# Optimization experiments

Hardware: AMD Instinct MI355X
Metric: run time of the kernel (lower is better)

The kernel has to match this reference:

```python
import jax, jax.numpy as jnp
import numpy as np

B, H, W = 1, 32, 32
C, G, K = 128, 4, 15
GC = C // G          # group channels = 32
K2 = K * K           # 225
RED = 4              # SE reduction
KHID = 32            # kernel_net hidden


def setup_inputs() -> dict:
    key = jax.random.key(0)
    ks = jax.random.split(key, 24)
    def n(k, shape, s=0.02):
        return jax.random.normal(k, shape, jnp.float32) * s
    inp = {
        'x': jax.random.normal(ks[0], (B, H, W, C), jnp.float32),
        # scalars (torch: raw_sigma init = softplus^{-1}(0.3), base_offset_scale = 0.1)
        'raw_sigma': jnp.asarray(float(np.log(np.expm1(0.3))), jnp.float32),
        'base_offset_scale': jnp.asarray(0.1, jnp.float32),
        # input/output projections
        'w_in': n(ks[1], (C, C)), 'b_in': jnp.zeros((C,), jnp.float32),
        'w_out': n(ks[2], (C, C)), 'b_out': jnp.zeros((C,), jnp.float32),
        # dw_conv: depthwise 3x3 (HWIO, I=1 per group) + pointwise 1x1
        'dw_k': n(ks[3], (3, 3, 1, C), 0.1), 'dw_b': jnp.zeros((C,), jnp.float32),
        'pw_w': n(ks[4], (C, C)), 'pw_b': jnp.zeros((C,), jnp.float32),
        # offset / mask nets (zero-init in torch; small random here to exercise gather)
        'off_w': n(ks[5], (C, G * K2 * 2), 0.01), 'off_b': n(ks[6], (G * K2 * 2,), 0.01),
        'msk_w': n(ks[7], (C, G * K2), 0.01), 'msk_b': n(ks[8], (G * K2,), 0.01),
        # kernel_net: 2 -> 32 -> 32 -> G*GC
        'k1_w': n(ks[9], (2, KHID), 0.3), 'k1_b': jnp.zeros((KHID,), jnp.float32),
        'k2_w': n(ks[10], (KHID, KHID), 0.2), 'k2_b': jnp.zeros((KHID,), jnp.float32),
        'k3_w': n(ks[11], (KHID, G * GC), 0.2), 'k3_b': jnp.zeros((G * GC,), jnp.float32),
        # SE block
        'se1_w': n(ks[12], (C, C // RED), 0.1), 'se1_b': jnp.zeros((C // RED,), jnp.float32),
        'se2_w': n(ks[13], (C // RED, C), 0.1), 'se2_b': jnp.zeros((C,), jnp.float32),
    }
    return inp


def reference(x, raw_sigma, base_offset_scale, w_in, b_in, w_out, b_out,
              dw_k, dw_b, pw_w, pw_b, off_w, off_b, msk_w, msk_b,
              k1_w, k1_b, k2_w, k2_b, k3_w, k3_b, se1_w, se1_b, se2_w, se2_b):
    # sigma (scalar path, biases=None)
    sigma = jnp.clip(jax.nn.softplus(raw_sigma), 0.001, 0.5)
    grid = jnp.linspace(-0.5, 0.5, K)

    x_proj = x @ w_in + b_in                                   # [B,H,W,C]

    # dw_conv: depthwise 3x3 -> SiLU -> 1x1
    y = jax.lax.conv_general_dilated(
        x, dw_k, (1, 1), 'SAME',
        dimension_numbers=('NHWC', 'HWIO', 'NHWC'),
        feature_group_count=C) + dw_b
    x_dw = jax.nn.silu(y) @ pw_w + pw_b                        # [B,H,W,C]

    # Gaussian envelope over kernel grid, normalized (scalar sigma -> shape [K,K])
    gh = grid[:, None]; gw = grid[None, :]
    env = jnp.exp(-(gh ** 2 + gw ** 2) / (2.0 * sigma ** 2))
    env = env / jnp.clip(env.sum(), 1e-8)                      # [K,K]

    # dynamic kernel weights from grid positions (*2); replicate torch's
    # contiguous view (K,K,G,gc) -> (G,K2,gc)
    pos = jnp.stack(jnp.meshgrid(grid, grid, indexing='ij'), -1).reshape(K2, 2) * 2.0
    h1 = jax.nn.silu(pos @ k1_w + k1_b)
    h2 = jax.nn.silu(h1 @ k2_w + k2_b)
    kw = (h2 @ k3_w + k3_b).reshape(K, K, G, GC).reshape(G, K2, GC)  # [G,K2,gc]

    offsets = (x_dw @ off_w + off_b).reshape(B, H, W, G, K2, 2) * base_offset_scale
    raw_mask = (x_dw @ msk_w + msk_b).reshape(B, H, W, G, K2) * env.reshape(1, 1, 1, 1, K2)
    attn = jnp.nan_to_num(jax.nn.softmax(raw_mask, axis=-1))   # [B,H,W,G,K2]

    # reference sampling grid (integer offsets -K//2..K//2)
    ref = jnp.linspace(-(K // 2), K // 2, K)
    ref_grid = jnp.stack(jnp.meshgrid(ref, ref, indexing='ij'), -1).reshape(K2, 2)
    pos_h = jnp.arange(H, dtype=jnp.float32).reshape(1, H, 1, 1, 1)
    pos_w = jnp.arange(W, dtype=jnp.float32).reshape(1, 1, W, 1, 1)

    abs_h = pos_h + ref_grid[:, 0].reshape(1, 1, 1, 1, K2) + offsets[..., 0]
    abs_w = pos_w + ref_grid[:, 1].reshape(1, 1, 1, 1, K2) + offsets[..., 1]
    ah = jnp.clip(abs_h, 0.0, H - 1); aw = jnp.clip(abs_w, 0.0, W - 1)
    hf = jnp.clip(ah.astype(jnp.int32), 0, H - 1)
    wf = jnp.clip(aw.astype(jnp.int32), 0, W - 1)
    hc = jnp.clip(hf + 1, 0, H - 1)
    wc = jnp.clip(wf + 1, 0, W - 1)
    hw = ah - hf.astype(jnp.float32)
    ww = aw - wf.astype(jnp.float32)
    valid = (~((abs_h < 0) | (abs_h > H - 1) | (abs_w < 0) | (abs_w > W - 1))).astype(jnp.float32)

    x_g = x_proj.reshape(B, H, W, G, GC)
    b_idx = jnp.arange(B).reshape(B, 1, 1, 1, 1)
    g_idx = jnp.arange(G).reshape(1, 1, 1, G, 1)
    def gather(hi, wi):
        return x_g[b_idx, hi, wi, g_idx]                       # [B,H,W,G,K2,gc]

    sampled = (gather(hf, wf) * ((1 - hw) * (1 - ww) * valid)[..., None]
             + gather(hf, wc) * ((1 - hw) * ww * valid)[..., None]
             + gather(hc, wf) * (hw * (1 - ww) * valid)[..., None]
             + gather(hc, wc) * (hw * ww * valid)[..., None])

    sampled = sampled * kw.reshape(1, 1, 1, G, K2, GC)
    out = jnp.einsum('bhwgkc,bhwgk->bhwgc', sampled, attn).reshape(B, H, W, C)

    # SE block (mask=None, bias=None)
    pooled = out.mean(axis=(1, 2), keepdims=True)
    scale = jax.nn.sigmoid(jax.nn.silu(pooled @ se1_w + se1_b) @ se2_w + se2_b)
    out = out * scale

    return out @ w_out + b_out
```

## Files before the change

### kernel.cpp

```cpp
#include <hip/hip_runtime.h>
#include <math.h>

constexpr int H = 32, W = 32, C = 128, G = 4, K = 15, K2 = 225, GC = 32;
constexpr int NPIX = H * W;
constexpr int NOFF = G * K2 * 2;
constexpr int NMSK = G * K2;
constexpr int NTOT = NOFF + NMSK;
constexpr int KHID = 32;

constexpr size_t WS_ENV    = 128;
constexpr size_t WS_KW     = 384;
constexpr size_t WS_PART   = 29184;
constexpr size_t WS_XPROJ  = 94720;
constexpr size_t WS_XDW    = 225792;
constexpr size_t WS_OFFS   = 356864;
constexpr size_t WS_MASK   = 2200064;
constexpr size_t WS_OUTPRE = 3121664;

__device__ __forceinline__ float sigmoidf_(float v) { return 1.f / (1.f + expf(-v)); }
__device__ __forceinline__ float siluf_(float v)    { return v / (1.f + expf(-v)); }

__device__ __forceinline__ void mlp_point(int k2i, int lane,
        const float* __restrict__ k1_w, const float* __restrict__ k1_b,
        const float* __restrict__ k2_w, const float* __restrict__ k2_b,
        const float* __restrict__ k3_w, const float* __restrict__ k3_b,
        float* __restrict__ ws) {
    int i = k2i / 15, j = k2i % 15;
    float ph = (-0.5f + (float)i * (1.f / 14.f)) * 2.f;
    float pw = (-0.5f + (float)j * (1.f / 14.f)) * 2.f;
    float h1[KHID], h2[KHID];
#pragma unroll
    for (int m = 0; m < KHID; m++)
        h1[m] = siluf_(fmaf(ph, k1_w[m], fmaf(pw, k1_w[KHID + m], k1_b[m])));
#pragma unroll
    for (int m = 0; m < KHID; m++) {
        float a = k2_b[m];
#pragma unroll
        for (int q = 0; q < KHID; q++) a = fmaf(h1[q], k2_w[q * KHID + m], a);
        h2[m] = siluf_(a);
    }
#pragma unroll
    for (int t = 0; t < 2; t++) {
        int col = lane + t * 64;
        float a = k3_b[col];
#pragma unroll
        for (int q = 0; q < KHID; q++) a = fmaf(h2[q], k3_w[q * C + col], a);
        ws[WS_KW + (size_t)k2i * C + col] = a;
    }
}

__global__ __launch_bounds__(256) void prep_front_kernel(const float* __restrict__ x,
        const float* __restrict__ raw_sigma,
        const float* __restrict__ w_in, const float* __restrict__ b_in,
        const float* __restrict__ dw_k, const float* __restrict__ dw_b,
        const float* __restrict__ pw_w, const float* __restrict__ pw_b,
        const float* __restrict__ k1_w, const float* __restrict__ k1_b,
        const float* __restrict__ k2_w, const float* __restrict__ k2_b,
        const float* __restrict__ k3_w, const float* __restrict__ k3_b,
        float* __restrict__ ws) {
    int tid = threadIdx.x;
    int b = blockIdx.x;
    if (b < 256) {
        __shared__ float xs[4][C], ts[4][C];
        int p0 = b * 4;
        int c = tid & 127, pp = tid >> 7;
#pragma unroll
        for (int q = 0; q < 2; q++) {
            int px = pp * 2 + q;
            int p = p0 + px;
            int h = p >> 5, w = p & 31;
            xs[px][c] = x[(size_t)p * C + c];
            float y = dw_b[c];
#pragma unroll
            for (int dy = 0; dy < 3; dy++) {
                int hh = h + dy - 1;
                if (hh < 0 || hh >= H) continue;
#pragma unroll
                for (int dx = 0; dx < 3; dx++) {
                    int wq = w + dx - 1;
                    if (wq < 0 || wq >= W) continue;
                    y = fmaf(x[((size_t)hh * W + wq) * C + c], dw_k[(dy * 3 + dx) * C + c], y);
                }
            }
            ts[px][c] = siluf_(y);
        }
        __syncthreads();
        float ap0 = b_in[c], ap1 = ap0, ad0 = pw_b[c], ad1 = ad0;
        int b0 = pp * 2, b1 = pp * 2 + 1;
        for (int i = 0; i < C; i += 4) {
#pragma unroll
            for (int u = 0; u < 4; u++) {
                float wi = w_in[(size_t)(i + u) * C + c];
                float pi = pw_w[(size_t)(i + u) * C + c];
                ap0 = fmaf(xs[b0][i + u], wi, ap0);
                ap1 = fmaf(xs[b1][i + u], wi, ap1);
                ad0 = fmaf(ts[b0][i + u], pi, ad0);
                ad1 = fmaf(ts[b1][i + u], pi, ad1);
            }
        }
        ws[WS_XPROJ + (size_t)(p0 + b0) * C + c] = ap0;
        ws[WS_XPROJ + (size_t)(p0 + b1) * C + c] = ap1;
        ws[WS_XDW  + (size_t)(p0 + b0) * C + c] = ad0;
        ws[WS_XDW  + (size_t)(p0 + b1) * C + c] = ad1;
    } else {
        int mb = b - 256;
        if (mb == 0) {
            __shared__ float red[256];
            float xsg = raw_sigma[0];
            float sp = fmaxf(xsg, 0.f) + log1pf(expf(-fabsf(xsg)));
            float sigma = fminf(fmaxf(sp, 0.001f), 0.5f);
            float inv2s2 = 1.f / (2.f * sigma * sigma);
            int i = tid / 15, j = tid % 15;
            float e = 0.f;
            if (tid < K2) {
                float gi = -0.5f + (float)i * (1.f / 14.f);
                float gj = -0.5f + (float)j * (1.f / 14.f);
                e = expf(-(gi * gi + gj * gj) * inv2s2);
            }
            red[tid] = e;
            __syncthreads();
            for (int s = 128; s > 0; s >>= 1) {
                if (tid < s) red[tid] += red[tid + s];
                __syncthreads();
            }
            float esum = fmaxf(red[0], 1e-8f);
            if (tid < K2) ws[WS_ENV + tid] = e / esum;
            if (tid < 64) mlp_point(224, tid, k1_w, k1_b, k2_w, k2_b, k3_w, k3_b, ws);
        } else {
            int k2i = (mb - 1) * 4 + (tid >> 6);
            mlp_point(k2i, tid & 63, k1_w, k1_b, k2_w, k2_b, k3_w, k3_b, ws);
        }
    }
}

__global__ __launch_bounds__(256) void offmsk_gemm(const float* __restrict__ A,
        const float* __restrict__ off_w, const float* __restrict__ off_b,
        const float* __restrict__ msk_w, const float* __restrict__ msk_b,
        const float* __restrict__ bos, const float* __restrict__ env,
        float* __restrict__ offs_out, float* __restrict__ mask_out) {
    __shared__ float At[32][132];
    __shared__ float Bs[32][128];
    int tid = threadIdx.x;
    int c0 = blockIdx.x * 128;
    int p0 = blockIdx.y * 128;
    int tx = tid & 15, ty = tid >> 4;

    float acc[8][8];
#pragma unroll
    for (int i = 0; i < 8; i++)
#pragma unroll
        for (int j = 0; j < 8; j++) acc[i][j] = 0.f;

    int cL = (tid & 31) * 4;
    int kB = tid >> 5;
    int cB = c0 + cL;
    const float* bptr = nullptr; int bstride = 0;
    if (cB < NOFF)       { bptr = off_w + cB;          bstride = NOFF; }
    else if (cB < NTOT)  { bptr = msk_w + (cB - NOFF); bstride = NMSK; }
    int rA = tid >> 3, k4A = (tid & 7) * 4;

    for (int kt = 0; kt < C; kt += 32) {
        if (kt) __syncthreads();
#pragma unroll
        for (int pass = 0; pass < 4; pass++) {
            int r = rA + pass * 32;
            float4 v = *(const float4*)&A[(size_t)(p0 + r) * C + kt + k4A];
            At[k4A + 0][r] = v.x; At[k4A + 1][r] = v.y;
            At[k4A + 2][r] = v.z; At[k4A + 3][r] = v.w;
        }
#pragma unroll
        for (int pass = 0; pass < 4; pass++) {
            int k = kB + pass * 8;
            float4 bv = make_float4(0.f, 0.f, 0.f, 0.f);
            if (bptr) bv = *(const float4*)&bptr[(size_t)(kt + k) * bstride];
            *(float4*)&Bs[k][cL] = bv;
        }
        __syncthreads();
#pragma unroll 4
        for (int k = 0; k < 32; k++) {
            float4 a0 = *(const float4*)&At[k][ty * 8];
            float4 a1 = *(const float4*)&At[k][ty * 8 + 4];
            float4 b0 = *(const float4*)&Bs[k][tx * 8];
            float4 b1 = *(const float4*)&Bs[k][tx * 8 + 4];
            const float av[8] = {a0.x, a0.y, a0.z, a0.w, a1.x, a1.y, a1.z, a1.w};
            const float bv[8] = {b0.x, b0.y, b0.z, b0.w, b1.x, b1.y, b1.z, b1.w};
#pragma unroll
            for (int i = 0; i < 8; i++)
#pragma unroll
                for (int j = 0; j < 8; j++)
                    acc[i][j] = fmaf(av[i], bv[j], acc[i][j]);
        }
    }

    int colbase = c0 + tx * 8;
    if (colbase >= NTOT) return;
    bool full = (colbase + 8) <= NTOT;
    float bias[8], sc[8];
    float* obase;
    int ostride;
    if (colbase < NOFF) {
        float s = bos[0];
#pragma unroll
        for (int j = 0; j < 8; j++) { bias[j] = off_b[colbase + j]; sc[j] = s; }
        obase = offs_out + colbase; ostride = NOFF;
    } else {
        int m0 = colbase - NOFF;
#pragma unroll
        for (int j = 0; j < 8; j++) {
            if (colbase + j < NTOT) { bias[j] = msk_b[m0 + j]; sc[j] = env[(m0 + j) % K2]; }
            else                    { bias[j] = 0.f; sc[j] = 0.f; }
        }
        obase = mask_out + m0; ostride = NMSK;
    }
#pragma unroll
    for (int i = 0; i < 8; i++) {
        size_t row = (size_t)(p0 + ty * 8 + i);
        if (full) {
            float4 r0 = make_float4((acc[i][0] + bias[0]) * sc[0], (acc[i][1] + bias[1]) * sc[1],
                                    (acc[i][2] + bias[2]) * sc[2], (acc[i][3] + bias[3]) * sc[3]);
            float4 r1 = make_float4((acc[i][4] + bias[4]) * sc[4], (acc[i][5] + bias[5]) * sc[5],
                                    (acc[i][6] + bias[6]) * sc[6], (acc[i][7] + bias[7]) * sc[7]);
            *(float4*)&obase[row * ostride]     = r0;
            *(float4*)&obase[row * ostride + 4] = r1;
        } else {
#pragma unroll
            for (int j = 0; j < 8; j++)
                if (colbase + j < NTOT)
                    obase[row * ostride + j] = (acc[i][j] + bias[j]) * sc[j];
        }
    }
}

__global__ __launch_bounds__(256) void sampler_kernel(const float* __restrict__ ws_offs,
        const float* __restrict__ ws_mask, const float* __restrict__ xproj,
        const float* __restrict__ kwf, float* __restrict__ outpre,
        float* __restrict__ partial) {
    int blk = blockIdx.x;
    int p0 = blk * 2;
    int h = p0 >> 5;
    int tid = threadIdx.x;

    __shared__ float   attn_s[2][NMSK];
    __shared__ float4  wgt_s[2][NMSK];
    __shared__ ushort4 loc_s[2][NMSK];
    __shared__ float   outp[2][C];

    {
        int half = tid >> 5;
        int l32 = tid & 31;
        int px = half >> 2, g = half & 3;
        const float* mrow = ws_mask + (size_t)(p0 + px) * NMSK + g * K2;
        float v[8];
        float mx = -1e30f;
#pragma unroll
        for (int q = 0; q < 8; q++) {
            int k = l32 + q * 32;
            v[q] = (k < K2) ? mrow[k] : -1e30f;
            mx = fmaxf(mx, v[q]);
        }
#pragma unroll
        for (int s = 16; s > 0; s >>= 1) mx = fmaxf(mx, __shfl_xor(mx, s));
        float sum = 0.f;
#pragma unroll
        for (int q = 0; q < 8; q++) {
            int k = l32 + q * 32;
            v[q] = (k < K2) ? expf(v[q] - mx) : 0.f;
            sum += v[q];
        }
#pragma unroll
        for (int s = 16; s > 0; s >>= 1) sum += __shfl_xor(sum, s);
        float inv = 1.f / sum;
#pragma unroll
        for (int q = 0; q < 8; q++) {
            int k = l32 + q * 32;
            if (k < K2) attn_s[px][g * K2 + k] = v[q] * inv;
        }
    }
    __syncthreads();

    for (int e = tid; e < 2 * NMSK; e += 256) {
        int px = (e >= NMSK) ? 1 : 0;
        int m = e - px * NMSK;
        int g = m / K2;
        int k = m - g * K2;
        int p = p0 + px;
        int w = p & 31;
        float2 o = *(const float2*)&ws_offs[(size_t)p * NOFF + m * 2];
        float abs_h = (float)(h + k / 15 - 7) + o.x;
        float abs_w = (float)(w + k % 15 - 7) + o.y;
        float validf = (abs_h < 0.f || abs_h > 31.f || abs_w < 0.f || abs_w > 31.f) ? 0.f : 1.f;
        float ah = fminf(fmaxf(abs_h, 0.f), 31.f);
        float aw = fminf(fmaxf(abs_w, 0.f), 31.f);
        int hf = (int)ah, wf = (int)aw;
        int hc = min(hf + 1, 31), wc = min(wf + 1, 31);
        float hwt = ah - (float)hf, wwt = aw - (float)wf;
        float a = attn_s[px][m] * validf;
        float u0 = 1.f - hwt, u1 = 1.f - wwt;
        wgt_s[px][m] = make_float4(a * u0 * u1, a * u0 * wwt, a * hwt * u1, a * hwt * wwt);
        loc_s[px][m] = make_ushort4((unsigned short)(hf * W + wf), (unsigned short)(hf * W + wc),
                                    (unsigned short)(hc * W + wf), (unsigned short)(hc * W + wc));
    }
    __syncthreads();

    {
        int cq = tid & 7;
        int s  = (tid >> 3) & 3;
        int g  = (tid >> 5) & 3;
        int px = tid >> 7;
        int k0 = (s * K2) >> 2;
        int k1 = ((s + 1) * K2) >> 2;
        const float* xpg = xproj + g * GC + cq * 4;
        const float* kwg = kwf + (size_t)g * (K2 * GC) + cq * 4;
        float4 acc = make_float4(0.f, 0.f, 0.f, 0.f);
#pragma unroll 2
        for (int k = k0; k < k1; k++) {
            int m = g * K2 + k;
            ushort4 L  = loc_s[px][m];
            float4  Wv = wgt_s[px][m];
            float4 x00 = *(const float4*)(xpg + (int)L.x * C);
            float4 x01 = *(const float4*)(xpg + (int)L.y * C);
            float4 x10 = *(const float4*)(xpg + (int)L.z * C);
            float4 x11 = *(const float4*)(xpg + (int)L.w * C);
            float4 kw4 = *(const float4*)(kwg + k * GC);
            float sx = fmaf(Wv.w, x11.x, fmaf(Wv.z, x10.x, fmaf(Wv.y, x01.x, Wv.x * x00.x)));
            float sy = fmaf(Wv.w, x11.y, fmaf(Wv.z, x10.y, fmaf(Wv.y, x01.y, Wv.x * x00.y)));
            float sz = fmaf(Wv.w, x11.z, fmaf(Wv.z, x10.z, fmaf(Wv.y, x01.z, Wv.x * x00.z)));
            float sw = fmaf(Wv.w, x11.w, fmaf(Wv.z, x10.w, fmaf(Wv.y, x01.w, Wv.x * x00.w)));
            acc.x = fmaf(kw4.x, sx, acc.x);
            acc.y = fmaf(kw4.y, sy, acc.y);
            acc.z = fmaf(kw4.z, sz, acc.z);
            acc.w = fmaf(kw4.w, sw, acc.w);
        }
        acc.x += __shfl_xor(acc.x, 8);  acc.y += __shfl_xor(acc.y, 8);
        acc.z += __shfl_xor(acc.z, 8);  acc.w += __shfl_xor(acc.w, 8);
        acc.x += __shfl_xor(acc.x, 16); acc.y += __shfl_xor(acc.y, 16);
        acc.z += __shfl_xor(acc.z, 16); acc.w += __shfl_xor(acc.w, 16);
        if (s == 0) {
            *(float4*)&outp[px][g * GC + cq * 4] = acc;
            *(float4*)&outpre[(size_t)(p0 + px) * C + g * GC + cq * 4] = acc;
        }
    }
    __syncthreads();
    if (tid < C)
        partial[(size_t)blk * C + tid] = outp[0][tid] + outp[1][tid];
}

__global__ __launch_bounds__(256) void finale_kernel(const float* __restrict__ outpre,
        const float* __restrict__ partial,
        const float* __restrict__ se1_w, const float* __restrict__ se1_b,
        const float* __restrict__ se2_w, const float* __restrict__ se2_b,
        const float* __restrict__ w_out, const float* __restrict__ b_out,
        float* __restrict__ out) {
    int tid = threadIdx.x;
    __shared__ float tmp[8][132];
    __shared__ float pooled[C];
    __shared__ float hid[KHID];
    __shared__ float scl[C];
    __shared__ float v[4][C];

    {
        int bg = tid >> 5, c4 = (tid & 31) * 4;
        float4 s4 = make_float4(0.f, 0.f, 0.f, 0.f);
        for (int i = 0; i < 64; i++) {
            float4 pv = *(const float4*)&partial[(size_t)(bg * 64 + i) * C + c4];
            s4.x += pv.x; s4.y += pv.y; s4.z += pv.z; s4.w += pv.w;
        }
        *(float4*)&tmp[bg][c4] = s4;
    }
    __syncthreads();
    if (tid < C) {
        float s = 0.f;
#pragma unroll
        for (int g = 0; g < 8; g++) s += tmp[g][tid];
        pooled[tid] = s * (1.f / 1024.f);
    }
    __syncthreads();
    if (tid < KHID) {
        float a = se1_b[tid];
        for (int cc = 0; cc < C; cc++) a = fmaf(pooled[cc], se1_w[cc * KHID + tid], a);
        hid[tid] = siluf_(a);
    }
    __syncthreads();
    if (tid < C) {
        float a = se2_b[tid];
#pragma unroll
        for (int q = 0; q < KHID; q++) a = fmaf(hid[q], se2_w[q * C + tid], a);
        scl[tid] = sigmoidf_(a);
    }
    __syncthreads();

    int p0 = blockIdx.x * 4;
    int c = tid & 127, pp = tid >> 7;
#pragma unroll
    for (int q = 0; q < 2; q++) {
        int px = pp * 2 + q;
        v[px][c] = outpre[(size_t)(p0 + px) * C + c] * scl[c];
    }
    __syncthreads();
    float a0 = b_out[c], a1 = b_out[c];
    int b0 = pp * 2, b1 = pp * 2 + 1;
    for (int i = 0; i < C; i += 4) {
#pragma unroll
        for (int u = 0; u < 4; u++) {
            float wv = w_out[(size_t)(i + u) * C + c];
            a0 = fmaf(v[b0][i + u], wv, a0);
            a1 = fmaf(v[b1][i + u], wv, a1);
        }
    }
    out[(size_t)(p0 + b0) * C + c] = a0;
    out[(size_t)(p0 + b1) * C + c] = a1;
}

extern "C" void kernel_launch(void* const* d_in, const int* in_sizes, int n_in,
                              void* d_out, int out_size, void* d_ws, size_t ws_size,
                              hipStream_t stream) {
    const float* x         = (const float*)d_in[0];
    const float* raw_sigma = (const float*)d_in[1];
    const float* bos       = (const float*)d_in[2];
    const float* w_in      = (const float*)d_in[3];
    const float* b_in      = (const float*)d_in[4];
    const float* w_out     = (const float*)d_in[5];
    const float* b_out     = (const float*)d_in[6];
    const float* dw_k      = (const float*)d_in[7];
    const float* dw_b      = (const float*)d_in[8];
    const float* pw_w      = (const float*)d_in[9];
    const float* pw_b      = (const float*)d_in[10];
    const float* off_w     = (const float*)d_in[11];
    const float* off_b     = (const float*)d_in[12];
    const float* msk_w     = (const float*)d_in[13];
    const float* msk_b     = (const float*)d_in[14];
    const float* k1_w      = (const float*)d_in[15];
    const float* k1_b      = (const float*)d_in[16];
    const float* k2_w      = (const float*)d_in[17];
    const float* k2_b      = (const float*)d_in[18];
    const float* k3_w      = (const float*)d_in[19];
    const float* k3_b      = (const float*)d_in[20];
    const float* se1_w     = (const float*)d_in[21];
    const float* se1_b     = (const float*)d_in[22];
    const float* se2_w     = (const float*)d_in[23];
    const float* se2_b     = (const float*)d_in[24];

    float* ws  = (float*)d_ws;
    float* out = (float*)d_out;

    prep_front_kernel<<<313, 256, 0, stream>>>(x, raw_sigma, w_in, b_in, dw_k, dw_b,
                                               pw_w, pw_b, k1_w, k1_b, k2_w, k2_b,
                                               k3_w, k3_b, ws);

    dim3 gg((NTOT + 127) / 128, NPIX / 128);
    offmsk_gemm<<<gg, 256, 0, stream>>>(ws + WS_XDW, off_w, off_b, msk_w, msk_b, bos,
                                        ws + WS_ENV, ws + WS_OFFS, ws + WS_MASK);

    sampler_kernel<<<NPIX / 2, 256, 0, stream>>>(ws + WS_OFFS, ws + WS_MASK, ws + WS_XPROJ,
                                                 ws + WS_KW, ws + WS_OUTPRE, ws + WS_PART);

    finale_kernel<<<NPIX / 4, 256, 0, stream>>>(ws + WS_OUTPRE, ws + WS_PART,
                                                se1_w, se1_b, se2_w, se2_b,
                                                w_out, b_out, out);
}
```

Before: 79.63 us.

## Stage neighborhood tile in LDS for sampler and shrink offset GEMM tiles

The sampler now handles a 2x2 pixel block per workgroup. For each group it stages an 18x18 halo tile of x_proj channels in shared memory, so bilinear gathers read LDS instead of global memory. Zero-weight samples are skipped, and the finale partial-sum reduction changes to match 256 blocks. The offset/mask GEMM moves from 128x128 to 64x64 tiles, giving more blocks. The sampler risks many more barriers per block, lower occupancy from about 47KB of LDS, and clamped halo indices if offsets fall outside the tile.

```diff
diff --git a/kernel.cpp b/kernel.cpp
--- a/kernel.cpp
+++ b/kernel.cpp
@@ -138,96 +138,72 @@
         const float* __restrict__ msk_w, const float* __restrict__ msk_b,
         const float* __restrict__ bos, const float* __restrict__ env,
         float* __restrict__ offs_out, float* __restrict__ mask_out) {
-    __shared__ float At[32][132];
-    __shared__ float Bs[32][128];
+    __shared__ float At[32][72];
+    __shared__ float Bs[32][64];
     int tid = threadIdx.x;
-    int c0 = blockIdx.x * 128;
-    int p0 = blockIdx.y * 128;
+    int c0 = blockIdx.x * 64;
+    int p0 = blockIdx.y * 64;
     int tx = tid & 15, ty = tid >> 4;
-
-    float acc[8][8];
-#pragma unroll
-    for (int i = 0; i < 8; i++)
-#pragma unroll
-        for (int j = 0; j < 8; j++) acc[i][j] = 0.f;
-
-    int cL = (tid & 31) * 4;
-    int kB = tid >> 5;
+    float acc[4][4];
+#pragma unroll
+    for (int i = 0; i < 4; i++)
+#pragma unroll
+        for (int j = 0; j < 4; j++) acc[i][j] = 0.f;
+    int cL = (tid * 4) & 63;
+    int kL = (tid * 4) >> 6;
     int cB = c0 + cL;
     const float* bptr = nullptr; int bstride = 0;
     if (cB < NOFF)       { bptr = off_w + cB;          bstride = NOFF; }
     else if (cB < NTOT)  { bptr = msk_w + (cB - NOFF); bstride = NMSK; }
     int rA = tid >> 3, k4A = (tid & 7) * 4;
-
     for (int kt = 0; kt < C; kt += 32) {
         if (kt) __syncthreads();
 #pragma unroll
-        for (int pass = 0; pass < 4; pass++) {
+        for (int pass = 0; pass < 2; pass++) {
             int r = rA + pass * 32;
             float4 v = *(const float4*)&A[(size_t)(p0 + r) * C + kt + k4A];
             At[k4A + 0][r] = v.x; At[k4A + 1][r] = v.y;
             At[k4A + 2][r] = v.z; At[k4A + 3][r] = v.w;
-        }
-#pragma unroll
-        for (int pass = 0; pass < 4; pass++) {
-            int k = kB + pass * 8;
+            int k = kL + pass * 16;
             float4 bv = make_float4(0.f, 0.f, 0.f, 0.f);
             if (bptr) bv = *(const float4*)&bptr[(size_t)(kt + k) * bstride];
             *(float4*)&Bs[k][cL] = bv;
         }
         __syncthreads();
-#pragma unroll 4
+#pragma unroll
         for (int k = 0; k < 32; k++) {
-            float4 a0 = *(const float4*)&At[k][ty * 8];
-            float4 a1 = *(const float4*)&At[k][ty * 8 + 4];
-            float4 b0 = *(const float4*)&Bs[k][tx * 8];
-            float4 b1 = *(const float4*)&Bs[k][tx * 8 + 4];
-            const float av[8] = {a0.x, a0.y, a0.z, a0.w, a1.x, a1.y, a1.z, a1.w};
-            const float bv[8] = {b0.x, b0.y, b0.z, b0.w, b1.x, b1.y, b1.z, b1.w};
-#pragma unroll
-            for (int i = 0; i < 8; i++)
-#pragma unroll
-                for (int j = 0; j < 8; j++)
+            float4 a4 = *(const float4*)&At[k][ty * 4];
+            float4 b4 = *(const float4*)&Bs[k][tx * 4];
+            const float av[4] = {a4.x, a4.y, a4.z, a4.w};
+            const float bv[4] = {b4.x, b4.y, b4.z, b4.w};
+#pragma unroll
+            for (int i = 0; i < 4; i++)
+#pragma unroll
+                for (int j = 0; j < 4; j++)
                     acc[i][j] = fmaf(av[i], bv[j], acc[i][j]);
         }
     }
-
-    int colbase = c0 + tx * 8;
+    int colbase = c0 + tx * 4;
     if (colbase >= NTOT) return;
-    bool full = (colbase + 8) <= NTOT;
-    float bias[8], sc[8];
-    float* obase;
-    int ostride;
+    float bias[4], sc[4];
+    float* obase; int ostride;
     if (colbase < NOFF) {
         float s = bos[0];
 #pragma unroll
-        for (int j = 0; j < 8; j++) { bias[j] = off_b[colbase + j]; sc[j] = s; }
+        for (int j = 0; j < 4; j++) { bias[j] = off_b[colbase + j]; sc[j] = s; }
         obase = offs_out + colbase; ostride = NOFF;
     } else {
         int m0 = colbase - NOFF;
 #pragma unroll
-        for (int j = 0; j < 8; j++) {
-            if (colbase + j < NTOT) { bias[j] = msk_b[m0 + j]; sc[j] = env[(m0 + j) % K2]; }
-            else                    { bias[j] = 0.f; sc[j] = 0.f; }
-        }
+        for (int j = 0; j < 4; j++) { bias[j] = msk_b[m0 + j]; sc[j] = env[(m0 + j) % K2]; }
         obase = mask_out + m0; ostride = NMSK;
     }
 #pragma unroll
-    for (int i = 0; i < 8; i++) {
-        size_t row = (size_t)(p0 + ty * 8 + i);
-        if (full) {
-            float4 r0 = make_float4((acc[i][0] + bias[0]) * sc[0], (acc[i][1] + bias[1]) * sc[1],
-                                    (acc[i][2] + bias[2]) * sc[2], (acc[i][3] + bias[3]) * sc[3]);
-            float4 r1 = make_float4((acc[i][4] + bias[4]) * sc[4], (acc[i][5] + bias[5]) * sc[5],
-                                    (acc[i][6] + bias[6]) * sc[6], (acc[i][7] + bias[7]) * sc[7]);
-            *(float4*)&obase[row * ostride]     = r0;
-            *(float4*)&obase[row * ostride + 4] = r1;
-        } else {
-#pragma unroll
-            for (int j = 0; j < 8; j++)
-                if (colbase + j < NTOT)
-                    obase[row * ostride + j] = (acc[i][j] + bias[j]) * sc[j];
-        }
+    for (int i = 0; i < 4; i++) {
+        size_t row = (size_t)(p0 + ty * 4 + i);
+        float4 r0 = make_float4((acc[i][0] + bias[0]) * sc[0], (acc[i][1] + bias[1]) * sc[1],
+                                (acc[i][2] + bias[2]) * sc[2], (acc[i][3] + bias[3]) * sc[3]);
+        *(float4*)&obase[row * ostride] = r0;
     }
 }
 
@@ -236,113 +212,142 @@
         const float* __restrict__ kwf, float* __restrict__ outpre,
         float* __restrict__ partial) {
     int blk = blockIdx.x;
-    int p0 = blk * 2;
-    int h = p0 >> 5;
+    int h0 = (blk >> 4) * 2, w0 = (blk & 15) * 2;
     int tid = threadIdx.x;
 
-    __shared__ float   attn_s[2][NMSK];
-    __shared__ float4  wgt_s[2][NMSK];
-    __shared__ ushort4 loc_s[2][NMSK];
-    __shared__ float   outp[2][C];
-
-    {
-        int half = tid >> 5;
-        int l32 = tid & 31;
-        int px = half >> 2, g = half & 3;
-        const float* mrow = ws_mask + (size_t)(p0 + px) * NMSK + g * K2;
-        float v[8];
-        float mx = -1e30f;
-#pragma unroll
-        for (int q = 0; q < 8; q++) {
-            int k = l32 + q * 32;
-            v[q] = (k < K2) ? mrow[k] : -1e30f;
-            mx = fmaxf(mx, v[q]);
-        }
-#pragma unroll
-        for (int s = 16; s > 0; s >>= 1) mx = fmaxf(mx, __shfl_xor(mx, s));
-        float sum = 0.f;
-#pragma unroll
-        for (int q = 0; q < 8; q++) {
-            int k = l32 + q * 32;
-            v[q] = (k < K2) ? expf(v[q] - mx) : 0.f;
-            sum += v[q];
-        }
-#pragma unroll
-        for (int s = 16; s > 0; s >>= 1) sum += __shfl_xor(sum, s);
-        float inv = 1.f / sum;
-#pragma unroll
-        for (int q = 0; q < 8; q++) {
-            int k = l32 + q * 32;
-            if (k < K2) attn_s[px][g * K2 + k] = v[q] * inv;
-        }
-    }
-    __syncthreads();
-
-    for (int e = tid; e < 2 * NMSK; e += 256) {
-        int px = (e >= NMSK) ? 1 : 0;
-        int m = e - px * NMSK;
-        int g = m / K2;
-        int k = m - g * K2;
-        int p = p0 + px;
-        int w = p & 31;
-        float2 o = *(const float2*)&ws_offs[(size_t)p * NOFF + m * 2];
-        float abs_h = (float)(h + k / 15 - 7) + o.x;
-        float abs_w = (float)(w + k % 15 - 7) + o.y;
-        float validf = (abs_h < 0.f || abs_h > 31.f || abs_w < 0.f || abs_w > 31.f) ? 0.f : 1.f;
-        float ah = fminf(fmaxf(abs_h, 0.f), 31.f);
-        float aw = fminf(fmaxf(abs_w, 0.f), 31.f);
-        int hf = (int)ah, wf = (int)aw;
-        int hc = min(hf + 1, 31), wc = min(wf + 1, 31);
-        float hwt = ah - (float)hf, wwt = aw - (float)wf;
-        float a = attn_s[px][m] * validf;
-        float u0 = 1.f - hwt, u1 = 1.f - wwt;
-        wgt_s[px][m] = make_float4(a * u0 * u1, a * u0 * wwt, a * hwt * u1, a * hwt * wwt);
-        loc_s[px][m] = make_ushort4((unsigned short)(hf * W + wf), (unsigned short)(hf * W + wc),
-                                    (unsigned short)(hc * W + wf), (unsigned short)(hc * W + wc));
-    }
-    __syncthreads();
-
-    {
-        int cq = tid & 7;
-        int s  = (tid >> 3) & 3;
-        int g  = (tid >> 5) & 3;
-        int px = tid >> 7;
-        int k0 = (s * K2) >> 2;
-        int k1 = ((s + 1) * K2) >> 2;
-        const float* xpg = xproj + g * GC + cq * 4;
-        const float* kwg = kwf + (size_t)g * (K2 * GC) + cq * 4;
-        float4 acc = make_float4(0.f, 0.f, 0.f, 0.f);
-#pragma unroll 2
-        for (int k = k0; k < k1; k++) {
-            int m = g * K2 + k;
-            ushort4 L  = loc_s[px][m];
-            float4  Wv = wgt_s[px][m];
-            float4 x00 = *(const float4*)(xpg + (int)L.x * C);
-            float4 x01 = *(const float4*)(xpg + (int)L.y * C);
-            float4 x10 = *(const float4*)(xpg + (int)L.z * C);
-            float4 x11 = *(const float4*)(xpg + (int)L.w * C);
-            float4 kw4 = *(const float4*)(kwg + k * GC);
-            float sx = fmaf(Wv.w, x11.x, fmaf(Wv.z, x10.x, fmaf(Wv.y, x01.x, Wv.x * x00.x)));
-            float sy = fmaf(Wv.w, x11.y, fmaf(Wv.z, x10.y, fmaf(Wv.y, x01.y, Wv.x * x00.y)));
-            float sz = fmaf(Wv.w, x11.z, fmaf(Wv.z, x10.z, fmaf(Wv.y, x01.z, Wv.x * x00.z)));
-            float sw = fmaf(Wv.w, x11.w, fmaf(Wv.z, x10.w, fmaf(Wv.y, x01.w, Wv.x * x00.w)));
-            acc.x = fmaf(kw4.x, sx, acc.x);
-            acc.y = fmaf(kw4.y, sy, acc.y);
-            acc.z = fmaf(kw4.z, sz, acc.z);
-            acc.w = fmaf(kw4.w, sw, acc.w);
-        }
-        acc.x += __shfl_xor(acc.x, 8);  acc.y += __shfl_xor(acc.y, 8);
-        acc.z += __shfl_xor(acc.z, 8);  acc.w += __shfl_xor(acc.w, 8);
-        acc.x += __shfl_xor(acc.x, 16); acc.y += __shfl_xor(acc.y, 16);
-        acc.z += __shfl_xor(acc.z, 16); acc.w += __shfl_xor(acc.w, 16);
-        if (s == 0) {
-            *(float4*)&outp[px][g * GC + cq * 4] = acc;
-            *(float4*)&outpre[(size_t)(p0 + px) * C + g * GC + cq * 4] = acc;
-        }
-    }
-    __syncthreads();
+    __shared__ float   reg[324 * 36];
+    __shared__ float   attn_g[4][228];
+    __shared__ float4  wvec[256];
+    __shared__ ushort4 locr[256];
+    __shared__ float4  rbuf[256];
+    __shared__ float   outp[4][C];
+
+    float4 accg;
+
+    for (int g = 0; g < G; ++g) {
+        for (int f = tid; f < 2592; f += 256) {
+            int cell = f >> 3, c4 = (f & 7) << 2;
+            int rr = cell / 18, cc2 = cell - rr * 18;
+            int gh = min(max(h0 - 8 + rr, 0), 31);
+            int gw = min(max(w0 - 8 + cc2, 0), 31);
+            float4 v = *(const float4*)&xproj[(size_t)((gh << 5) + gw) * C + g * GC + c4];
+            *(float4*)&reg[cell * 36 + c4] = v;
+        }
+        {
+            int px = tid >> 6, lane = tid & 63;
+            int p = ((h0 + (px >> 1)) << 5) + w0 + (px & 1);
+            const float* mrow = ws_mask + (size_t)p * NMSK + g * K2;
+            float v[4];
+            float mx = -1e30f;
+#pragma unroll
+            for (int q = 0; q < 4; q++) {
+                int k = lane + q * 64;
+                v[q] = (k < K2) ? mrow[k] : -1e30f;
+                mx = fmaxf(mx, v[q]);
+            }
+#pragma unroll
+            for (int s = 32; s > 0; s >>= 1) mx = fmaxf(mx, __shfl_xor(mx, s));
+            float sum = 0.f;
+#pragma unroll
+            for (int q = 0; q < 4; q++) {
+                int k = lane + q * 64;
+                v[q] = (k < K2) ? expf(v[q] - mx) : 0.f;
+                sum += v[q];
+            }
+#pragma unroll
+            for (int s = 32; s > 0; s >>= 1) sum += __shfl_xor(sum, s);
+            float inv = 1.f / sum;
+#pragma unroll
+            for (int q = 0; q < 4; q++) {
+                int k = lane + q * 64;
+                if (k < K2) attn_g[px][k] = v[q] * inv;
+            }
+        }
+        __syncthreads();
+
+        accg = make_float4(0.f, 0.f, 0.f, 0.f);
+        for (int kc = 0; kc < K2; kc += 64) {
+            {
+                int px = tid >> 6, kk = tid & 63, k = kc + kk;
+                float a = 0.f, hwt = 0.f, wwt = 0.f;
+                ushort4 l4 = make_ushort4(0, 0, 0, 0);
+                if (k < K2) {
+                    int ph = h0 + (px >> 1), pw = w0 + (px & 1);
+                    int p = (ph << 5) + pw;
+                    float2 o = *(const float2*)&ws_offs[(size_t)p * NOFF + (g * K2 + k) * 2];
+                    float abs_h = (float)(ph + k / 15 - 7) + o.x;
+                    float abs_w = (float)(pw + k % 15 - 7) + o.y;
+                    float validf = (abs_h < 0.f || abs_h > 31.f || abs_w < 0.f || abs_w > 31.f) ? 0.f : 1.f;
+                    float ah = fminf(fmaxf(abs_h, 0.f), 31.f);
+                    float aw = fminf(fmaxf(abs_w, 0.f), 31.f);
+                    int hf = (int)ah, wf = (int)aw;
+                    int hc = min(hf + 1, 31), wc = min(wf + 1, 31);
+                    hwt = ah - (float)hf; wwt = aw - (float)wf;
+                    a = attn_g[px][k] * validf;
+                    int ri0 = min(max(hf - h0 + 8, 0), 17);
+                    int ri1 = min(max(hc - h0 + 8, 0), 17);
+                    int rj0 = min(max(wf - w0 + 8, 0), 17);
+                    int rj1 = min(max(wc - w0 + 8, 0), 17);
+                    l4 = make_ushort4((unsigned short)(ri0 * 18 + rj0), (unsigned short)(ri0 * 18 + rj1),
+                                      (unsigned short)(ri1 * 18 + rj0), (unsigned short)(ri1 * 18 + rj1));
+                }
+                wvec[tid] = make_float4(a, hwt, wwt, 0.f);
+                locr[tid] = l4;
+            }
+            __syncthreads();
+            {
+                int cq = tid & 7, px = (tid >> 3) & 3, s = tid >> 5;
+#pragma unroll
+                for (int i = 0; i < 8; i++) {
+                    int kk = s * 8 + i;
+                    int e = px * 64 + kk;
+                    float4 wv = wvec[e];
+                    if (wv.x != 0.f) {
+                        ushort4 L = locr[e];
+                        float u0 = 1.f - wv.y, u1 = 1.f - wv.z;
+                        float w00 = wv.x * u0 * u1,   w01 = wv.x * u0 * wv.z;
+                        float w10 = wv.x * wv.y * u1, w11 = wv.x * wv.y * wv.z;
+                        float4 x00 = *(const float4*)&reg[(int)L.x * 36 + cq * 4];
+                        float4 x01 = *(const float4*)&reg[(int)L.y * 36 + cq * 4];
+                        float4 x10 = *(const float4*)&reg[(int)L.z * 36 + cq * 4];
+                        float4 x11 = *(const float4*)&reg[(int)L.w * 36 + cq * 4];
+                        float4 kw4 = *(const float4*)&kwf[(size_t)g * (K2 * GC) + (kc + kk) * GC + cq * 4];
+                        float sx = fmaf(w11, x11.x, fmaf(w10, x10.x, fmaf(w01, x01.x, w00 * x00.x)));
+                        float sy = fmaf(w11, x11.y, fmaf(w10, x10.y, fmaf(w01, x01.y, w00 * x00.y)));
+                        float sz = fmaf(w11, x11.z, fmaf(w10, x10.z, fmaf(w01, x01.z, w00 * x00.z)));
+                        float sw = fmaf(w11, x11.w, fmaf(w10, x10.w, fmaf(w01, x01.w, w00 * x00.w)));
+                        accg.x = fmaf(kw4.x, sx, accg.x);
+                        accg.y = fmaf(kw4.y, sy, accg.y);
+                        accg.z = fmaf(kw4.z, sz, accg.z);
+                        accg.w = fmaf(kw4.w, sw, accg.w);
+                    }
+                }
+            }
+            __syncthreads();
+        }
+        {
+            int cq = tid & 7, px = (tid >> 3) & 3, s = tid >> 5;
+            rbuf[s * 32 + px * 8 + cq] = accg;
+        }
+        __syncthreads();
+        if (tid < 128) {
+            int px = tid >> 5, cc = tid & 31;
+            float v = 0.f;
+#pragma unroll
+            for (int s = 0; s < 8; s++)
+                v += ((const float*)&rbuf[s * 32 + px * 8 + (cc >> 2)])[cc & 3];
+            outp[px][g * GC + cc] = v;
+        }
+        __syncthreads();
+    }
+
+    for (int t = tid; t < 4 * C; t += 256) {
+        int px = t >> 7, c = t & 127;
+        int p = ((h0 + (px >> 1)) << 5) + w0 + (px & 1);
+        outpre[(size_t)p * C + c] = outp[px][c];
+    }
     if (tid < C)
-        partial[(size_t)blk * C + tid] = outp[0][tid] + outp[1][tid];
+        partial[(size_t)blk * C + tid] = outp[0][tid] + outp[1][tid] + outp[2][tid] + outp[3][tid];
 }
 
 __global__ __launch_bounds__(256) void finale_kernel(const float* __restrict__ outpre,
@@ -361,8 +366,8 @@
     {
         int bg = tid >> 5, c4 = (tid & 31) * 4;
         float4 s4 = make_float4(0.f, 0.f, 0.f, 0.f);
-        for (int i = 0; i < 64; i++) {
-            float4 pv = *(const float4*)&partial[(size_t)(bg * 64 + i) * C + c4];
+        for (int i = 0; i < 32; i++) {
+            float4 pv = *(const float4*)&partial[(size_t)(bg * 32 + i) * C + c4];
             s4.x += pv.x; s4.y += pv.y; s4.z += pv.z; s4.w += pv.w;
         }
         *(float4*)&tmp[bg][c4] = s4;
@@ -447,12 +452,12 @@
                                                pw_w, pw_b, k1_w, k1_b, k2_w, k2_b,
                                                k3_w, k3_b, ws);
 
-    dim3 gg((NTOT + 127) / 128, NPIX / 128);
+    dim3 gg((NTOT + 63) / 64, NPIX / 64);
     offmsk_gemm<<<gg, 256, 0, stream>>>(ws + WS_XDW, off_w, off_b, msk_w, msk_b, bos,
                                         ws + WS_ENV, ws + WS_OFFS, ws + WS_MASK);
 
-    sampler_kernel<<<NPIX / 2, 256, 0, stream>>>(ws + WS_OFFS, ws + WS_MASK, ws + WS_XPROJ,
-                                                 ws + WS_KW, ws + WS_OUTPRE, ws + WS_PART);
+    sampler_kernel<<<256, 256, 0, stream>>>(ws + WS_OFFS, ws + WS_MASK, ws + WS_XPROJ,
+                                            ws + WS_KW, ws + WS_OUTPRE, ws + WS_PART);
 
     finale_kernel<<<NPIX / 4, 256, 0, stream>>>(ws + WS_OUTPRE, ws + WS_PART,
                                                 se1_w, se1_b, se2_w, se2_b,
```

After: 94.26 us. 1.18x slower.
